# Kernel optimization log

Hardware: AMD Instinct MI355X
Metric: run time of the kernel (lower is better)

## Reference

```python
import jax, jax.numpy as jnp
import numpy as np

DT_MIN, DT_MAX = 1e-3, 0.1
DT_RANK, D_STATE = 64, 16


def setup_inputs() -> dict:
    key = jax.random.key(0)
    ks = jax.random.split(key, 8)
    B, L, D_MODEL, D_INNER = 2, 4096, 1024, 2048
    s = 0.02
    return {
        "x": jax.random.normal(ks[0], (B, L, D_MODEL), jnp.float32),
        "W_in": jax.random.normal(ks[1], (D_MODEL, 2 * D_INNER), jnp.float32) * s,
        "W_xproj": jax.random.normal(ks[2], (D_INNER, DT_RANK + 2 * D_STATE), jnp.float32) * s,
        "W_dt": jax.random.normal(ks[3], (DT_RANK, D_INNER), jnp.float32) * s,
        "b_dt": jax.random.normal(ks[4], (D_INNER,), jnp.float32) * s,
        "A_log": jnp.log(jax.random.uniform(ks[5], (D_INNER, D_STATE), jnp.float32) + 0.5),
        "D": jnp.ones((D_INNER,), jnp.float32),
        "W_out": jax.random.normal(ks[6], (D_INNER, D_MODEL), jnp.float32) * s,
    }


def _selective_scan(xp, delta, A, Bm, Cm):
    # xp, delta: [B, L, d_inner]; Bm, Cm: [B, L, d_state]; A: [d_inner, d_state]
    batch, L, d_inner = xp.shape
    d_state = A.shape[1]

    def step(h, inp):
        x_t, dt_t, B_t, C_t = inp  # [B,di], [B,di], [B,ds], [B,ds]
        A_bar = 1.0 + A[None] * dt_t[..., None]            # [B, di, ds]
        B_bar = B_t[:, None, :] * dt_t[..., None]          # [B, di, ds]
        h = A_bar * h + B_bar * x_t[..., None]             # [B, di, ds]
        y_t = jnp.sum(C_t[:, None, :] * h, axis=-1)        # [B, di]
        return h, y_t

    h0 = jnp.zeros((batch, d_inner, d_state), xp.dtype)
    xs = (
        jnp.swapaxes(xp, 0, 1),
        jnp.swapaxes(delta, 0, 1),
        jnp.swapaxes(Bm, 0, 1),
        jnp.swapaxes(Cm, 0, 1),
    )
    _, ys = jax.lax.scan(step, h0, xs)  # ys: [L, B, d_inner]
    return jnp.swapaxes(ys, 0, 1)


def reference(x, W_in, W_xproj, W_dt, b_dt, A_log, D, W_out):
    xz = x @ W_in
    xp, z = jnp.split(xz, 2, axis=-1)                      # [B,L,d_inner] each
    x_dbl = xp @ W_xproj
    dlt, Bm, Cm = jnp.split(x_dbl, [DT_RANK, DT_RANK + D_STATE], axis=-1)
    delta = jnp.clip(jax.nn.softplus(dlt @ W_dt + b_dt), DT_MIN, DT_MAX)
    A = -jnp.exp(A_log)
    y = _selective_scan(xp, delta, A, Bm, Cm)
    y = y + D[None, None, :] * xp
    y = y * jax.nn.silu(z)
    return y @ W_out
```

## Files before the change

### kernel.cpp

```cpp
#include <hip/hip_runtime.h>
#include <cstdint>
#include <cstddef>

typedef unsigned short u16;
typedef __attribute__((ext_vector_type(8))) short bf16x8;
typedef __attribute__((ext_vector_type(4))) float f32x4;

__device__ __forceinline__ float bf2f(u16 u) {
  unsigned v = ((unsigned)u) << 16;
  return __builtin_bit_cast(float, v);
}
__device__ __forceinline__ u16 f2bf(float f) {
  unsigned u = __builtin_bit_cast(unsigned, f);
  u = (u + 0x7FFFu + ((u >> 16) & 1u)) >> 16;
  return (u16)u;
}

__device__ __forceinline__ void gload16(const void* g, void* l) {
  __builtin_amdgcn_global_load_lds(
      (const __attribute__((address_space(1))) void*)g,
      (__attribute__((address_space(3))) void*)l,
      16, 0, 0);
}

__device__ __forceinline__ int swz(int lb) { return lb ^ (((lb >> 7) & 7) << 4); }

__global__ __launch_bounds__(256) void f32_to_bf16_kernel(
    const float* __restrict__ in, u16* __restrict__ out, int n) {
  int i = (blockIdx.x * 256 + threadIdx.x) * 4;
  if (i < n) {
    float4 v = *(const float4*)(in + i);
    ushort4 o;
    o.x = f2bf(v.x); o.y = f2bf(v.y); o.z = f2bf(v.z); o.w = f2bf(v.w);
    *(ushort4*)(out + i) = o;
  }
}

__global__ void transpose_f32_bf16T_kernel(
    const float* __restrict__ in, u16* __restrict__ out, int R, int C) {
  __shared__ float tile[32][33];
  const int bx = blockIdx.x * 32;
  const int by = blockIdx.y * 32;
  const int tx = threadIdx.x, ty = threadIdx.y;
#pragma unroll
  for (int i = 0; i < 32; i += 8)
    tile[ty + i][tx] = in[(size_t)(by + ty + i) * C + bx + tx];
  __syncthreads();
#pragma unroll
  for (int i = 0; i < 32; i += 8)
    out[(size_t)(bx + ty + i) * R + by + tx] = f2bf(tile[tx][ty + i]);
}

template <int BN, int EPI>
__global__ __launch_bounds__(512, 2) void gemm256(
    const u16* __restrict__ Ap, const u16* __restrict__ Btp,
    int M, int N, int K, int gx,
    void* __restrict__ o0, void* __restrict__ o1) {
  constexpr int NFR = BN / 64;
  constexpr int NFH = NFR / 2;
  constexpr int A_ISS = 4;
  constexpr int B_ISS = BN / 64;
  constexpr int WN = BN / 4;
  constexpr int BUFSZ = 32768 + BN * 128;
  __shared__ __align__(1024) char smem[2 * BUFSZ];

  const int tid = threadIdx.x;
  const int wid = tid >> 6, lane = tid & 63;
  const int wr = wid >> 2, wc = wid & 3;
  const int l16 = lane & 15, lk = lane >> 4;

  const int nwg = gridDim.x, bid = blockIdx.x;
  const int rb = (bid & 7) * (nwg >> 3) + (bid >> 3);
  const int bx = rb % gx, by = rb / gx;
  const int m0 = by * 256, n0 = bx * BN;

  const u16* gA[A_ISS];
  const u16* gB[B_ISS];
#pragma unroll
  for (int i = 0; i < A_ISS; ++i) {
    int pb = i * 8192 + tid * 16;
    int lb = swz(pb);
    gA[i] = Ap + (size_t)(m0 + (lb >> 7)) * K + ((lb & 127) >> 1);
  }
#pragma unroll
  for (int i = 0; i < B_ISS; ++i) {
    int pb = i * 8192 + tid * 16;
    int lb = swz(pb);
    gB[i] = Btp + (size_t)(n0 + (lb >> 7)) * K + ((lb & 127) >> 1);
  }

  auto stage = [&](int kt, int bb) {
    char* dst = smem + bb * BUFSZ + (wid << 10);
#pragma unroll
    for (int i = 0; i < A_ISS; ++i)
      gload16(gA[i] + kt * 64, dst + i * 8192);
#pragma unroll
    for (int i = 0; i < B_ISS; ++i)
      gload16(gB[i] + kt * 64, dst + 32768 + i * 8192);
  };

  auto offA = [&](int f, int kk) {
    int lb = (wr * 128 + f * 16 + l16) * 128 + kk * 64 + lk * 16;
    return swz(lb);
  };
  auto offB = [&](int n, int kk) {
    int lb = (wc * WN + n * 16 + l16) * 128 + kk * 64 + lk * 16;
    return swz(lb);
  };

  f32x4 acc[8][NFR];
#pragma unroll
  for (int f = 0; f < 8; ++f)
#pragma unroll
    for (int n = 0; n < NFR; ++n) {
      f32x4 z = {0.f, 0.f, 0.f, 0.f};
      acc[f][n] = z;
    }

  const int NT = K >> 6;
  stage(0, 0);
  stage(1, 1);

  for (int kt = 0; kt < NT; ++kt) {
    const char* bufA = smem + (kt & 1) * BUFSZ;
    const char* bufB = bufA + 32768;
    if (kt < NT - 1) {
      if constexpr (B_ISS == 4) asm volatile("s_waitcnt vmcnt(8)" ::: "memory");
      else                      asm volatile("s_waitcnt vmcnt(6)" ::: "memory");
    } else {
      asm volatile("s_waitcnt vmcnt(0)" ::: "memory");
    }
    __builtin_amdgcn_s_barrier();

    bf16x8 af[4][2], bh[2][NFH][2];
#pragma unroll
    for (int j = 0; j < 4; ++j)
#pragma unroll
      for (int kk = 0; kk < 2; ++kk)
        af[j][kk] = *(const bf16x8*)(bufA + offA(j, kk));
#pragma unroll
    for (int j = 0; j < NFH; ++j)
#pragma unroll
      for (int kk = 0; kk < 2; ++kk)
        bh[0][j][kk] = *(const bf16x8*)(bufB + offB(j, kk));
    __builtin_amdgcn_s_setprio(1);
#pragma unroll
    for (int j = 0; j < 4; ++j)
#pragma unroll
      for (int n2 = 0; n2 < NFH; ++n2)
#pragma unroll
        for (int kk = 0; kk < 2; ++kk)
          acc[j][n2] = __builtin_amdgcn_mfma_f32_16x16x32_bf16(
              af[j][kk], bh[0][n2][kk], acc[j][n2], 0, 0, 0);
    __builtin_amdgcn_s_setprio(0);
#pragma unroll
    for (int j = 0; j < NFH; ++j)
#pragma unroll
      for (int kk = 0; kk < 2; ++kk)
        bh[1][j][kk] = *(const bf16x8*)(bufB + offB(NFH + j, kk));
    __builtin_amdgcn_s_setprio(1);
#pragma unroll
    for (int j = 0; j < 4; ++j)
#pragma unroll
      for (int n2 = 0; n2 < NFH; ++n2)
#pragma unroll
        for (int kk = 0; kk < 2; ++kk)
          acc[j][NFH + n2] = __builtin_amdgcn_mfma_f32_16x16x32_bf16(
              af[j][kk], bh[1][n2][kk], acc[j][NFH + n2], 0, 0, 0);
    __builtin_amdgcn_s_setprio(0);
#pragma unroll
    for (int j = 0; j < 4; ++j)
#pragma unroll
      for (int kk = 0; kk < 2; ++kk)
        af[j][kk] = *(const bf16x8*)(bufA + offA(4 + j, kk));
    __builtin_amdgcn_s_setprio(1);
#pragma unroll
    for (int j = 0; j < 4; ++j)
#pragma unroll
      for (int n2 = 0; n2 < NFH; ++n2)
#pragma unroll
        for (int kk = 0; kk < 2; ++kk)
          acc[4 + j][NFH + n2] = __builtin_amdgcn_mfma_f32_16x16x32_bf16(
              af[j][kk], bh[1][n2][kk], acc[4 + j][NFH + n2], 0, 0, 0);
    __builtin_amdgcn_s_setprio(0);
    __builtin_amdgcn_s_setprio(1);
#pragma unroll
    for (int j = 0; j < 4; ++j)
#pragma unroll
      for (int n2 = 0; n2 < NFH; ++n2)
#pragma unroll
        for (int kk = 0; kk < 2; ++kk)
          acc[4 + j][n2] = __builtin_amdgcn_mfma_f32_16x16x32_bf16(
              af[j][kk], bh[0][n2][kk], acc[4 + j][n2], 0, 0, 0);
    __builtin_amdgcn_s_setprio(0);

    asm volatile("s_waitcnt lgkmcnt(0)" ::: "memory");
    __builtin_amdgcn_s_barrier();
    if (kt + 2 < NT) stage(kt + 2, kt & 1);
  }

#pragma unroll
  for (int f = 0; f < 8; ++f) {
#pragma unroll
    for (int n = 0; n < NFR; ++n) {
#pragma unroll
      for (int rr = 0; rr < 4; ++rr) {
        const int row = m0 + wr * 128 + f * 16 + lk * 4 + rr;
        const int col = n0 + wc * WN + n * 16 + l16;
        float v = acc[f][n][rr];
        if constexpr (EPI == 0) {
          if (col < 2048) {
            ((u16*)o0)[(size_t)row * 2048 + col] = f2bf(v);
          } else {
            float sv = v / (1.f + __expf(-v));
            ((u16*)o1)[(size_t)row * 2048 + (col - 2048)] = f2bf(sv);
          }
        } else {
          ((float*)o0)[(size_t)row * (size_t)N + col] = v;
        }
      }
    }
  }
}

template <int BN, int NR, int EPI>
__global__ __launch_bounds__(256) void gemm_bt(
    const u16* __restrict__ A, const u16* __restrict__ Bt,
    int M, int N, int K, int KS,
    void* __restrict__ o0, const float* __restrict__ bias) {
  constexpr int BM = 128, BK = 32, MR = 4;
  __shared__ __align__(16) u16 As[BM * BK];
  __shared__ __align__(16) u16 Bs[BN * BK];
  const int tid = threadIdx.x;
  const int wid = tid >> 6, lane = tid & 63;
  const int wr = wid >> 1, wc = wid & 1;
  const int m0 = blockIdx.y * BM, n0 = blockIdx.x * BN;
  const int l16 = lane & 15, lk = lane >> 4;

  f32x4 acc[MR][NR];
#pragma unroll
  for (int m = 0; m < MR; ++m)
#pragma unroll
    for (int n = 0; n < NR; ++n) {
      f32x4 z = {0.f, 0.f, 0.f, 0.f};
      acc[m][n] = z;
    }

  constexpr int CH_A = (BM * BK * 2) / 1024;
  constexpr int CH_B = (BN * BK * 2) / 1024;

  const int kbeg = blockIdx.z * KS, kend = kbeg + KS;
  for (int k0 = kbeg; k0 < kend; k0 += BK) {
    for (int c = wid; c < CH_A; c += 4) {
      int off = c * 1024 + lane * 16;
      int e = off >> 1;
      int m = e >> 5, kk = e & 31;
      gload16(A + (size_t)(m0 + m) * K + (k0 + kk), (char*)As + off);
    }
    for (int c = wid; c < CH_B; c += 4) {
      int off = c * 1024 + lane * 16;
      int e = off >> 1;
      int n = e >> 5, kk = e & 31;
      gload16(Bt + (size_t)(n0 + n) * K + (k0 + kk), (char*)Bs + off);
    }
    __syncthreads();
    bf16x8 af[MR], bfr[NR];
#pragma unroll
    for (int m = 0; m < MR; ++m)
      af[m] = *(const bf16x8*)(As + (wr * 64 + m * 16 + l16) * BK + lk * 8);
#pragma unroll
    for (int n = 0; n < NR; ++n)
      bfr[n] = *(const bf16x8*)(Bs + (wc * (NR * 16) + n * 16 + l16) * BK + lk * 8);
#pragma unroll
    for (int m = 0; m < MR; ++m)
#pragma unroll
      for (int n = 0; n < NR; ++n)
        acc[m][n] = __builtin_amdgcn_mfma_f32_16x16x32_bf16(af[m], bfr[n], acc[m][n], 0, 0, 0);
    __syncthreads();
  }

#pragma unroll
  for (int m = 0; m < MR; ++m) {
#pragma unroll
    for (int n = 0; n < NR; ++n) {
#pragma unroll
      for (int r = 0; r < 4; ++r) {
        const int row = m0 + wr * 64 + m * 16 + (lane >> 4) * 4 + r;
        const int col = n0 + wc * (NR * 16) + n * 16 + (lane & 15);
        float v = acc[m][n][r];
        if constexpr (EPI == 2) {
          v += bias[col];
          float sp = (v > 20.f) ? v : log1pf(__expf(v));
          sp = fminf(fmaxf(sp, 1e-3f), 0.1f);
          ((u16*)o0)[(size_t)row * 2048 + col] = f2bf(sp);
        } else {
          ((float*)o0)[((size_t)blockIdx.z * M + row) * 96 + col] = v;
        }
      }
    }
  }
}

__global__ __launch_bounds__(256) void reduce_xdbl(
    const float* __restrict__ part, u16* __restrict__ dlt,
    float* __restrict__ Bc, float* __restrict__ Cc) {
  int idx = blockIdx.x * 256 + threadIdx.x;
  int row = idx / 24, c4 = idx % 24;
  const float* p = part + (size_t)row * 96 + c4 * 4;
  f32x4 v = *(const f32x4*)p;
#pragma unroll
  for (int z = 1; z < 4; ++z)
    v += *(const f32x4*)(p + (size_t)z * 8192 * 96);
  int col = c4 * 4;
  if (col < 64) {
    ushort4 o;
    o.x = f2bf(v[0]); o.y = f2bf(v[1]); o.z = f2bf(v[2]); o.w = f2bf(v[3]);
    *(ushort4*)(dlt + (size_t)row * 64 + col) = o;
  } else if (col < 80) {
    *(f32x4*)(Bc + (size_t)row * 16 + (col - 64)) = v;
  } else {
    *(f32x4*)(Cc + (size_t)row * 16 + (col - 80)) = v;
  }
}

template <int TC>
__global__ __launch_bounds__(256) void scan_pass1(
    const u16* __restrict__ xp, const u16* __restrict__ dt,
    const float* __restrict__ Bc, const float* __restrict__ A_log,
    float* __restrict__ P, float* __restrict__ Q, int NC) {
  const int di = blockIdx.x * 256 + threadIdx.x;
  const int c = blockIdx.y, b = blockIdx.z;
  __shared__ __align__(16) float Bs[TC * 16];
  {
    const float* src = Bc + (size_t)(b * 4096 + c * TC) * 16;
    for (int i = threadIdx.x; i < TC * 4; i += 256)
      *(float4*)(Bs + i * 4) = *(const float4*)(src + i * 4);
  }
  float A[16], h[16], Pp[16];
#pragma unroll
  for (int s = 0; s < 16; ++s) {
    A[s] = -__expf(A_log[di * 16 + s]);
    h[s] = 0.f;
    Pp[s] = 1.f;
  }
  __syncthreads();
  size_t gidx = (size_t)(b * 4096 + c * TC) * 2048 + di;
  for (int t = 0; t < TC; ++t, gidx += 2048) {
    float xv = bf2f(xp[gidx]), dv = bf2f(dt[gidx]);
    float dvx = dv * xv;
#pragma unroll
    for (int q = 0; q < 4; ++q) {
      f32x4 bv = ((const f32x4*)(Bs + t * 16))[q];
#pragma unroll
      for (int j = 0; j < 4; ++j) {
        int s = q * 4 + j;
        float abar = fmaf(A[s], dv, 1.f);
        h[s] = fmaf(abar, h[s], bv[j] * dvx);
        Pp[s] *= abar;
      }
    }
  }
  const size_t obase = ((size_t)(b * NC + c) * 16) * 2048 + di;
#pragma unroll
  for (int s = 0; s < 16; ++s) {
    P[obase + (size_t)s * 2048] = Pp[s];
    Q[obase + (size_t)s * 2048] = h[s];
  }
}

__global__ __launch_bounds__(256) void scan_pass2(
    const float* __restrict__ P, const float* __restrict__ Q,
    float* __restrict__ Hin, int NC) {
  const int di = blockIdx.x * 256 + threadIdx.x;
  const int s = blockIdx.y, b = blockIdx.z;
  float hin = 0.f;
  const size_t idx0 = ((size_t)(b * NC) * 16 + s) * 2048 + di;
#pragma unroll 8
  for (int c = 0; c < NC; ++c) {
    size_t idx = idx0 + (size_t)c * (16 * 2048);
    Hin[idx] = hin;
    hin = fmaf(P[idx], hin, Q[idx]);
  }
}

template <int TC>
__global__ __launch_bounds__(256) void scan_pass3(
    const u16* __restrict__ xp, const u16* __restrict__ dt,
    const u16* __restrict__ zs, const float* __restrict__ Bc,
    const float* __restrict__ Cc, const float* __restrict__ A_log,
    const float* __restrict__ Dv, const float* __restrict__ Hin,
    u16* __restrict__ Y, int NC) {
  const int di = blockIdx.x * 256 + threadIdx.x;
  const int c = blockIdx.y, b = blockIdx.z;
  __shared__ __align__(16) float Bs[TC * 16], Cs[TC * 16];
  {
    const float* srcB = Bc + (size_t)(b * 4096 + c * TC) * 16;
    const float* srcC = Cc + (size_t)(b * 4096 + c * TC) * 16;
    for (int i = threadIdx.x; i < TC * 4; i += 256) {
      *(float4*)(Bs + i * 4) = *(const float4*)(srcB + i * 4);
      *(float4*)(Cs + i * 4) = *(const float4*)(srcC + i * 4);
    }
  }
  float A[16], h[16];
  const size_t hbase = ((size_t)(b * NC + c) * 16) * 2048 + di;
#pragma unroll
  for (int s = 0; s < 16; ++s) {
    A[s] = -__expf(A_log[di * 16 + s]);
    h[s] = Hin[hbase + (size_t)s * 2048];
  }
  const float Dg = Dv[di];
  __syncthreads();
  size_t gidx = (size_t)(b * 4096 + c * TC) * 2048 + di;
  for (int t = 0; t < TC; ++t, gidx += 2048) {
    float xv = bf2f(xp[gidx]), dv = bf2f(dt[gidx]), zv = bf2f(zs[gidx]);
    float dvx = dv * xv;
    float y = 0.f;
#pragma unroll
    for (int q = 0; q < 4; ++q) {
      f32x4 bv = ((const f32x4*)(Bs + t * 16))[q];
      f32x4 cv = ((const f32x4*)(Cs + t * 16))[q];
#pragma unroll
      for (int j = 0; j < 4; ++j) {
        int s = q * 4 + j;
        float abar = fmaf(A[s], dv, 1.f);
        h[s] = fmaf(abar, h[s], bv[j] * dvx);
        y = fmaf(cv[j], h[s], y);
      }
    }
    float yo = fmaf(Dg, xv, y) * zv;
    Y[gidx] = f2bf(yo);
  }
}

extern "C" void kernel_launch(void* const* d_in, const int* in_sizes, int n_in,
                              void* d_out, int out_size, void* d_ws, size_t ws_size,
                              hipStream_t stream) {
  (void)in_sizes; (void)n_in; (void)out_size; (void)ws_size;
  const float* x       = (const float*)d_in[0];
  const float* W_in    = (const float*)d_in[1];
  const float* W_xproj = (const float*)d_in[2];
  const float* W_dt    = (const float*)d_in[3];
  const float* b_dt    = (const float*)d_in[4];
  const float* A_log   = (const float*)d_in[5];
  const float* Dv      = (const float*)d_in[6];
  const float* W_out   = (const float*)d_in[7];
  float* out = (float*)d_out;

  constexpr size_t MB = 1ull << 20;
  char* ws = (char*)d_ws;
  constexpr size_t O_XP    = 0;
  constexpr size_t O_ZS    = 32 * MB;
  constexpr size_t O_DELTA = 64 * MB;
  constexpr size_t O_BC    = 96 * MB;
  constexpr size_t O_CC    = O_BC + 512 * 1024;
  constexpr size_t O_WOUTT = 97 * MB;
  constexpr size_t O_Y     = 101 * MB;
  constexpr size_t O_XB    = 133 * MB;
  constexpr size_t O_WINT  = 149 * MB;
  constexpr size_t O_WXT   = 157 * MB;
  constexpr size_t O_WDTT  = O_WXT + 393216;
  constexpr size_t O_DLT   = O_WDTT + 262144;
  constexpr size_t O_P     = 133 * MB;
  constexpr size_t O_Q     = 149 * MB;
  constexpr size_t O_HIN   = 165 * MB;
  constexpr size_t O_XDP   = O_P;

  u16* xb    = (u16*)(ws + O_XB);
  u16* WinT  = (u16*)(ws + O_WINT);
  u16* WxT   = (u16*)(ws + O_WXT);
  u16* WdtT  = (u16*)(ws + O_WDTT);
  u16* WoutT = (u16*)(ws + O_WOUTT);
  u16* xpb   = (u16*)(ws + O_XP);
  u16* zsb   = (u16*)(ws + O_ZS);
  u16* dltb  = (u16*)(ws + O_DLT);
  float* Bcf = (float*)(ws + O_BC);
  float* Ccf = (float*)(ws + O_CC);
  u16* delb  = (u16*)(ws + O_DELTA);
  u16* Yb    = (u16*)(ws + O_Y);
  float* Pf  = (float*)(ws + O_P);
  float* Qf  = (float*)(ws + O_Q);
  float* Hin = (float*)(ws + O_HIN);
  float* xdp = (float*)(ws + O_XDP);

  dim3 tb(32, 8);
  f32_to_bf16_kernel<<<8192 * 1024 / 1024, 256, 0, stream>>>(x, xb, 8192 * 1024);
  transpose_f32_bf16T_kernel<<<dim3(4096 / 32, 1024 / 32), tb, 0, stream>>>(W_in, WinT, 1024, 4096);
  transpose_f32_bf16T_kernel<<<dim3(96 / 32, 2048 / 32), tb, 0, stream>>>(W_xproj, WxT, 2048, 96);
  transpose_f32_bf16T_kernel<<<dim3(2048 / 32, 64 / 32), tb, 0, stream>>>(W_dt, WdtT, 64, 2048);
  transpose_f32_bf16T_kernel<<<dim3(1024 / 32, 2048 / 32), tb, 0, stream>>>(W_out, WoutT, 2048, 1024);

  gemm256<256, 0><<<512, 512, 0, stream>>>(
      xb, WinT, 8192, 4096, 1024, 16, xpb, zsb);
  gemm_bt<96, 3, 4><<<dim3(1, 8192 / 128, 4), 256, 0, stream>>>(
      xpb, WxT, 8192, 96, 2048, 512, xdp, nullptr);
  reduce_xdbl<<<8192 * 24 / 256, 256, 0, stream>>>(xdp, dltb, Bcf, Ccf);
  gemm_bt<128, 4, 2><<<dim3(2048 / 128, 8192 / 128, 1), 256, 0, stream>>>(
      dltb, WdtT, 8192, 2048, 64, 64, delb, b_dt);

  constexpr int NC = 64, TC = 64;
  scan_pass1<TC><<<dim3(8, NC, 2), 256, 0, stream>>>(
      xpb, delb, Bcf, A_log, Pf, Qf, NC);
  scan_pass2<<<dim3(8, 16, 2), 256, 0, stream>>>(Pf, Qf, Hin, NC);
  scan_pass3<TC><<<dim3(8, NC, 2), 256, 0, stream>>>(
      xpb, delb, zsb, Bcf, Ccf, A_log, Dv, Hin, Yb, NC);

  gemm256<128, 3><<<256, 512, 0, stream>>>(
      Yb, WoutT, 8192, 1024, 2048, 8, out, nullptr);
}
```

Baseline: 328.1 us.

## Interleave split global-to-LDS staging across MFMA phases in GEMM main loop

Splits the per-tile global-to-LDS loads for A and B into half-tile pieces and issues them between the four MFMA phases of each K iteration, rather than issuing a full tile stage at the end of the iteration. Barriers and lgkmcnt waits are added around each phase so that buffer regions are overwritten only after they are consumed. The intent is to overlap memory traffic with matrix math more evenly and reduce stalls at the iteration boundary. The cost is extra workgroup barriers per iteration and tighter ordering hazards on shared buffers.

```diff
diff --git a/kernel.cpp b/kernel.cpp
--- a/kernel.cpp
+++ b/kernel.cpp
@@ -58,10 +58,10 @@
     void* __restrict__ o0, void* __restrict__ o1) {
   constexpr int NFR = BN / 64;
   constexpr int NFH = NFR / 2;
-  constexpr int A_ISS = 4;
   constexpr int B_ISS = BN / 64;
   constexpr int WN = BN / 4;
-  constexpr int BUFSZ = 32768 + BN * 128;
+  constexpr int AREG = 32768;
+  constexpr int BUFSZ = AREG + BN * 128;
   __shared__ __align__(1024) char smem[2 * BUFSZ];
 
   const int tid = threadIdx.x;
@@ -74,38 +74,39 @@
   const int bx = rb % gx, by = rb / gx;
   const int m0 = by * 256, n0 = bx * BN;
 
-  const u16* gA[A_ISS];
+  const u16* gA[4];
   const u16* gB[B_ISS];
 #pragma unroll
-  for (int i = 0; i < A_ISS; ++i) {
-    int pb = i * 8192 + tid * 16;
-    int lb = swz(pb);
+  for (int i = 0; i < 4; ++i) {
+    int lb = swz(i * 8192 + tid * 16);
     gA[i] = Ap + (size_t)(m0 + (lb >> 7)) * K + ((lb & 127) >> 1);
   }
 #pragma unroll
   for (int i = 0; i < B_ISS; ++i) {
-    int pb = i * 8192 + tid * 16;
-    int lb = swz(pb);
+    int lb = swz(i * 8192 + tid * 16);
     gB[i] = Btp + (size_t)(n0 + (lb >> 7)) * K + ((lb & 127) >> 1);
   }
 
-  auto stage = [&](int kt, int bb) {
-    char* dst = smem + bb * BUFSZ + (wid << 10);
-#pragma unroll
-    for (int i = 0; i < A_ISS; ++i)
-      gload16(gA[i] + kt * 64, dst + i * 8192);
-#pragma unroll
-    for (int i = 0; i < B_ISS; ++i)
-      gload16(gB[i] + kt * 64, dst + 32768 + i * 8192);
+  auto stageA = [&](int kt, int h) {
+    char* dst = smem + (kt & 1) * BUFSZ + (wid << 10);
+    gload16(gA[2 * h] + kt * 64, dst + (2 * h) * 8192);
+    gload16(gA[2 * h + 1] + kt * 64, dst + (2 * h + 1) * 8192);
   };
+  auto stageB = [&](int kt, int h) {
+    char* dst = smem + (kt & 1) * BUFSZ + AREG + (wid << 10);
+    if constexpr (B_ISS == 4) {
+      gload16(gB[2 * h] + kt * 64, dst + (2 * h) * 8192);
+      gload16(gB[2 * h + 1] + kt * 64, dst + (2 * h + 1) * 8192);
+    } else {
+      gload16(gB[h] + kt * 64, dst + h * 8192);
+    }
+  };
 
   auto offA = [&](int f, int kk) {
-    int lb = (wr * 128 + f * 16 + l16) * 128 + kk * 64 + lk * 16;
-    return swz(lb);
+    return swz((wr * 128 + f * 16 + l16) * 128 + kk * 64 + lk * 16);
   };
   auto offB = [&](int n, int kk) {
-    int lb = (wc * WN + n * 16 + l16) * 128 + kk * 64 + lk * 16;
-    return swz(lb);
+    return swz((wc * WN + n * 16 + l16) * 128 + kk * 64 + lk * 16);
   };
 
   f32x4 acc[8][NFR];
@@ -118,21 +119,16 @@
     }
 
   const int NT = K >> 6;
-  stage(0, 0);
-  stage(1, 1);
+  stageA(0, 0); stageA(0, 1); stageB(0, 0); stageB(0, 1);
+  stageA(1, 0);
+  asm volatile("s_waitcnt vmcnt(2)" ::: "memory");
+  __builtin_amdgcn_s_barrier();
 
   for (int kt = 0; kt < NT; ++kt) {
     const char* bufA = smem + (kt & 1) * BUFSZ;
-    const char* bufB = bufA + 32768;
-    if (kt < NT - 1) {
-      if constexpr (B_ISS == 4) asm volatile("s_waitcnt vmcnt(8)" ::: "memory");
-      else                      asm volatile("s_waitcnt vmcnt(6)" ::: "memory");
-    } else {
-      asm volatile("s_waitcnt vmcnt(0)" ::: "memory");
-    }
-    __builtin_amdgcn_s_barrier();
-
+    const char* bufB = bufA + AREG;
     bf16x8 af[4][2], bh[2][NFH][2];
+
 #pragma unroll
     for (int j = 0; j < 4; ++j)
 #pragma unroll
@@ -143,6 +139,10 @@
 #pragma unroll
       for (int kk = 0; kk < 2; ++kk)
         bh[0][j][kk] = *(const bf16x8*)(bufB + offB(j, kk));
+    if (kt + 1 < NT) stageA(kt + 1, 1);
+    __builtin_amdgcn_s_barrier();
+    asm volatile("s_waitcnt lgkmcnt(0)" ::: "memory");
+    __builtin_amdgcn_sched_barrier(0);
     __builtin_amdgcn_s_setprio(1);
 #pragma unroll
     for (int j = 0; j < 4; ++j)
@@ -153,11 +153,17 @@
           acc[j][n2] = __builtin_amdgcn_mfma_f32_16x16x32_bf16(
               af[j][kk], bh[0][n2][kk], acc[j][n2], 0, 0, 0);
     __builtin_amdgcn_s_setprio(0);
+    __builtin_amdgcn_s_barrier();
+
 #pragma unroll
     for (int j = 0; j < NFH; ++j)
 #pragma unroll
       for (int kk = 0; kk < 2; ++kk)
         bh[1][j][kk] = *(const bf16x8*)(bufB + offB(NFH + j, kk));
+    if (kt + 1 < NT) stageB(kt + 1, 0);
+    __builtin_amdgcn_s_barrier();
+    asm volatile("s_waitcnt lgkmcnt(0)" ::: "memory");
+    __builtin_amdgcn_sched_barrier(0);
     __builtin_amdgcn_s_setprio(1);
 #pragma unroll
     for (int j = 0; j < 4; ++j)
@@ -168,11 +174,17 @@
           acc[j][NFH + n2] = __builtin_amdgcn_mfma_f32_16x16x32_bf16(
               af[j][kk], bh[1][n2][kk], acc[j][NFH + n2], 0, 0, 0);
     __builtin_amdgcn_s_setprio(0);
+    __builtin_amdgcn_s_barrier();
+
 #pragma unroll
     for (int j = 0; j < 4; ++j)
 #pragma unroll
       for (int kk = 0; kk < 2; ++kk)
         af[j][kk] = *(const bf16x8*)(bufA + offA(4 + j, kk));
+    if (kt + 1 < NT) stageB(kt + 1, 1);
+    __builtin_amdgcn_s_barrier();
+    asm volatile("s_waitcnt lgkmcnt(0)" ::: "memory");
+    __builtin_amdgcn_sched_barrier(0);
     __builtin_amdgcn_s_setprio(1);
 #pragma unroll
     for (int j = 0; j < 4; ++j)
@@ -183,6 +195,15 @@
           acc[4 + j][NFH + n2] = __builtin_amdgcn_mfma_f32_16x16x32_bf16(
               af[j][kk], bh[1][n2][kk], acc[4 + j][NFH + n2], 0, 0, 0);
     __builtin_amdgcn_s_setprio(0);
+    __builtin_amdgcn_s_barrier();
+
+    if (kt + 2 < NT) {
+      stageA(kt + 2, 0);
+      asm volatile("s_waitcnt vmcnt(2)" ::: "memory");
+    } else if (kt + 1 < NT) {
+      asm volatile("s_waitcnt vmcnt(0)" ::: "memory");
+    }
+    __builtin_amdgcn_s_barrier();
     __builtin_amdgcn_s_setprio(1);
 #pragma unroll
     for (int j = 0; j < 4; ++j)
@@ -193,10 +214,7 @@
           acc[4 + j][n2] = __builtin_amdgcn_mfma_f32_16x16x32_bf16(
               af[j][kk], bh[0][n2][kk], acc[4 + j][n2], 0, 0, 0);
     __builtin_amdgcn_s_setprio(0);
-
-    asm volatile("s_waitcnt lgkmcnt(0)" ::: "memory");
-    __builtin_amdgcn_s_barrier();
-    if (kt + 2 < NT) stage(kt + 2, kt & 1);
+    __builtin_amdgcn_s_barrier();
   }
 
 #pragma unroll
```

After: 329.9 us. About the same (+0.6%).
